# Optimization experiments

Measured on AMD Instinct MI355X. Metric: run time of the kernel, lower is better.

## Reference

```python
import jax, jax.numpy as jnp
import numpy as np

N_NODES = 50000
N_EDGES = 800000
D_IN = 256
H = 4
D_OUT = 64
NEG_SLOPE = 0.2


def setup_inputs() -> dict:
    key = jax.random.key(0)
    ks = jax.random.split(key, 6)
    feat = jax.random.normal(ks[0], (N_NODES, D_IN), dtype=jnp.float32)
    src = jax.random.randint(ks[1], (N_EDGES,), 0, N_NODES, dtype=jnp.int32)
    dst = jax.random.randint(ks[2], (N_EDGES,), 0, N_NODES, dtype=jnp.int32)
    # Glorot-ish scaled params
    W_src = jax.random.normal(ks[3], (H * D_OUT, D_IN), dtype=jnp.float32) * (1.0 / np.sqrt(D_IN))
    W_dst = jax.random.normal(ks[4], (H * D_OUT, D_IN), dtype=jnp.float32) * (1.0 / np.sqrt(D_IN))
    b_src = jnp.zeros((H * D_OUT,), dtype=jnp.float32)
    b_dst = jnp.zeros((H * D_OUT,), dtype=jnp.float32)
    attn = jax.random.normal(ks[5], (H, D_OUT), dtype=jnp.float32) * (1.0 / np.sqrt(D_OUT))
    return {"feat": feat, "src": src, "dst": dst, "W_src": W_src, "b_src": b_src,
            "W_dst": W_dst, "b_dst": b_dst, "attn": attn}


def reference(feat, src, dst, W_src, b_src, W_dst, b_dst, attn):
    n = feat.shape[0]
    h, d = attn.shape
    # node projections [N, H, D]
    feat_src = (feat @ W_src.T + b_src).reshape(n, h, d)
    feat_dst = (feat @ W_dst.T + b_dst).reshape(n, h, d)
    # edge-wise u + v, LeakyReLU  -> [E, H, D]
    e = jax.nn.leaky_relu(feat_src[src] + feat_dst[dst], negative_slope=NEG_SLOPE)
    # attention logits [E, H]
    score = jnp.einsum('ehd,hd->eh', e, attn)
    # edge softmax over incoming edges per dst node (numerically stable)
    m = jax.ops.segment_max(score, dst, num_segments=n)
    expv = jnp.exp(score - m[dst])
    denom = jax.ops.segment_sum(expv, dst, num_segments=n)
    a = expv / denom[dst]  # [E, H]
    # weighted scatter-sum of source features -> [N, H, D]
    out = jax.ops.segment_sum(feat_src[src] * a[:, :, None], dst, num_segments=n)
    return out
```

## Files before the change

### kernel.cpp

```cpp
#include <hip/hip_runtime.h>
#include <math.h>

#define N_DIN 256
#define N_COUT 256
#define NEG_SLOPE 0.2f
#define L2E 1.44269504f
#define CAP 64

#define BM 128
#define BN 256
#define BK 32
#define LDK 40

typedef _Float16 f16;
typedef f16 f16x2 __attribute__((ext_vector_type(2)));
typedef f16 f16x4 __attribute__((ext_vector_type(4)));
typedef f16 f16x8 __attribute__((ext_vector_type(8)));
typedef float f32x4 __attribute__((ext_vector_type(4)));
typedef float f32x8 __attribute__((ext_vector_type(8)));

__global__ __launch_bounds__(512) void proj(
    const float* __restrict__ feat,
    const float* __restrict__ Wsrc, const float* __restrict__ bsrc,
    const float* __restrict__ Wdst, const float* __restrict__ bdst,
    f16* __restrict__ fsrc_h, f16* __restrict__ fdst_h, int n)
{
    __shared__ f16 Al[BM * LDK];
    __shared__ f16 Bl[BN * LDK];

    const int t = threadIdx.x;
    const int lane = t & 63;
    const int w = t >> 6;
    const int wr = w >> 2, wc = w & 3;
    const int which = blockIdx.x & 1;
    const float* __restrict__ W    = which ? Wdst : Wsrc;
    const float* __restrict__ bias = which ? bdst : bsrc;
    f16* __restrict__ outp         = which ? fdst_h : fsrc_h;
    const int row0 = ((int)blockIdx.x >> 1) * BM;

    const int lr = lane & 15;
    const int kc = lane >> 4;

    const int arow = t >> 2;
    const int akof = (t & 3) * 8;
    const int bcol = t >> 1;
    const int bkof = (t & 1) * 16;
    const int agrow = row0 + arow;
    const bool aval = agrow < n;
    const float* __restrict__ fbase = &feat[(size_t)(aval ? agrow : 0) * N_DIN];
    const float* __restrict__ wbase = &W[(size_t)bcol * N_DIN];

    f32x4 acc[4][4] = {};

    for (int k0 = 0; k0 < N_DIN; k0 += BK) {
        {
            f16x8 v = {};
            if (aval) {
                const float* fp = fbase + k0 + akof;
                float4 u0 = *reinterpret_cast<const float4*>(fp);
                float4 u1 = *reinterpret_cast<const float4*>(fp + 4);
                v[0] = (f16)u0.x; v[1] = (f16)u0.y; v[2] = (f16)u0.z; v[3] = (f16)u0.w;
                v[4] = (f16)u1.x; v[5] = (f16)u1.y; v[6] = (f16)u1.z; v[7] = (f16)u1.w;
            }
            *reinterpret_cast<f16x8*>(&Al[arow * LDK + akof]) = v;
        }
        {
            const float* wp = wbase + k0 + bkof;
            float4 u0 = *reinterpret_cast<const float4*>(wp);
            float4 u1 = *reinterpret_cast<const float4*>(wp + 4);
            float4 u2 = *reinterpret_cast<const float4*>(wp + 8);
            float4 u3 = *reinterpret_cast<const float4*>(wp + 12);
            f16x8 v0, v1;
            v0[0] = (f16)u0.x; v0[1] = (f16)u0.y; v0[2] = (f16)u0.z; v0[3] = (f16)u0.w;
            v0[4] = (f16)u1.x; v0[5] = (f16)u1.y; v0[6] = (f16)u1.z; v0[7] = (f16)u1.w;
            v1[0] = (f16)u2.x; v1[1] = (f16)u2.y; v1[2] = (f16)u2.z; v1[3] = (f16)u2.w;
            v1[4] = (f16)u3.x; v1[5] = (f16)u3.y; v1[6] = (f16)u3.z; v1[7] = (f16)u3.w;
            *reinterpret_cast<f16x8*>(&Bl[bcol * LDK + bkof]) = v0;
            *reinterpret_cast<f16x8*>(&Bl[bcol * LDK + bkof + 8]) = v1;
        }
        __syncthreads();

        f16x8 a[4], b[4];
        #pragma unroll
        for (int nf = 0; nf < 4; ++nf)
            a[nf] = *reinterpret_cast<const f16x8*>(
                &Bl[(wc * 64 + nf * 16 + lr) * LDK + kc * 8]);
        #pragma unroll
        for (int m = 0; m < 4; ++m)
            b[m] = *reinterpret_cast<const f16x8*>(
                &Al[(wr * 64 + m * 16 + lr) * LDK + kc * 8]);
        #pragma unroll
        for (int nf = 0; nf < 4; ++nf)
            #pragma unroll
            for (int m = 0; m < 4; ++m)
                acc[nf][m] = __builtin_amdgcn_mfma_f32_16x16x32_f16(
                    a[nf], b[m], acc[nf][m], 0, 0, 0);
        __syncthreads();
    }

    #pragma unroll
    for (int nf = 0; nf < 4; ++nf) {
        const int cbase = wc * 64 + nf * 16 + kc * 4;
        const float4 bv = *reinterpret_cast<const float4*>(&bias[cbase]);
        #pragma unroll
        for (int m = 0; m < 4; ++m) {
            const int row = row0 + wr * 64 + m * 16 + lr;
            if (row < n) {
                f16x4 o;
                o[0] = (f16)(acc[nf][m][0] + bv.x);
                o[1] = (f16)(acc[nf][m][1] + bv.y);
                o[2] = (f16)(acc[nf][m][2] + bv.z);
                o[3] = (f16)(acc[nf][m][3] + bv.w);
                *reinterpret_cast<f16x4*>(&outp[(size_t)row * N_COUT + cbase]) = o;
            }
        }
    }
}


__global__ __launch_bounds__(1024) void histA(
    const int* __restrict__ dst, int* __restrict__ hist, int E, int NB, int NGRP)
{
    __shared__ int cnt[256];
    const int b = blockIdx.x, t = threadIdx.x;
    if (t < 256) cnt[t] = 0;
    __syncthreads();
    int i = b * 1024 + t;
    if (i < E) atomicAdd(&cnt[dst[i] >> 8], 1);
    __syncthreads();
    if (t < NGRP) hist[(size_t)t * NB + b] = cnt[t];
}

__global__ __launch_bounds__(1024) void scanA(
    int* __restrict__ hist, int* __restrict__ gtot, int NB)
{
    __shared__ int wsum[16];
    int* h = hist + (size_t)blockIdx.x * NB;
    const int t = threadIdx.x, lane = t & 63, wv = t >> 6;
    int v = (t < NB) ? h[t] : 0;
    int x = v;
    #pragma unroll
    for (int o = 1; o < 64; o <<= 1) {
        int y = __shfl_up(x, (unsigned)o);
        if (lane >= o) x += y;
    }
    if (lane == 63) wsum[wv] = x;
    __syncthreads();
    if (t < 16) {
        int s = wsum[t];
        #pragma unroll
        for (int o = 1; o < 16; o <<= 1) {
            int y = __shfl_up(s, (unsigned)o);
            if (t >= o) s += y;
        }
        wsum[t] = s;
    }
    __syncthreads();
    int wbase = wv ? wsum[wv - 1] : 0;
    if (t < NB) h[t] = wbase + x - v;
    if (t == 0) gtot[blockIdx.x] = wsum[15];
}

__global__ __launch_bounds__(256) void scanB(
    const int* __restrict__ gtot, int* __restrict__ gbase, int NGRP, int E)
{
    __shared__ int wsum[4];
    const int t = threadIdx.x, lane = t & 63, wv = t >> 6;
    int v = (t < NGRP) ? gtot[t] : 0;
    int x = v;
    #pragma unroll
    for (int o = 1; o < 64; o <<= 1) {
        int y = __shfl_up(x, (unsigned)o);
        if (lane >= o) x += y;
    }
    if (lane == 63) wsum[wv] = x;
    __syncthreads();
    if (t < 4) {
        int s = wsum[t];
        #pragma unroll
        for (int o = 1; o < 4; o <<= 1) {
            int y = __shfl_up(s, (unsigned)o);
            if (t >= o) s += y;
        }
        wsum[t] = s;
    }
    __syncthreads();
    int wbase = wv ? wsum[wv - 1] : 0;
    if (t < NGRP) gbase[t] = wbase + x - v;
    if (t == 0) gbase[NGRP] = E;
}

__global__ __launch_bounds__(1024) void partition(
    const int* __restrict__ src, const int* __restrict__ dst,
    const int* __restrict__ hist, const int* __restrict__ gbase,
    int* __restrict__ psrc, int* __restrict__ pdst, int E, int NB, int NGRP)
{
    __shared__ int cnt[256];
    const int b = blockIdx.x, t = threadIdx.x;
    if (t < 256) cnt[t] = 0;
    __syncthreads();
    int i = b * 1024 + t;
    if (i < E) {
        int d = dst[i];
        int s = src[i];
        int g = d >> 8;
        int lr = atomicAdd(&cnt[g], 1);
        int pos = gbase[g] + hist[(size_t)g * NB + b] + lr;
        pdst[pos] = d;
        psrc[pos] = s;
    }
}

__global__ __launch_bounds__(1024) void finebucket(
    const int* __restrict__ psrc, const int* __restrict__ pdst,
    const int* __restrict__ gbase, int* __restrict__ ssrc,
    int* __restrict__ deg, int n)
{
    __shared__ int cnt[256];
    const int g = blockIdx.x, t = threadIdx.x;
    if (t < 256) cnt[t] = 0;
    __syncthreads();
    const int beg = gbase[g], end = gbase[g + 1];
    for (int i = beg + t; i < end; i += 1024) {
        int d = pdst[i];
        int s = psrc[i];
        int r = atomicAdd(&cnt[d & 255], 1);
        if (r < CAP) ssrc[(size_t)d * CAP + r] = s;
    }
    __syncthreads();
    int d = (g << 8) + t;
    if (t < 256 && d < n) deg[d] = cnt[t];
}


template<int Q>
__device__ __forceinline__ void gat_batch(
    int e0, int i0m, int i1m,
    const f16* __restrict__ fsrc_h, int cb,
    f16x8 fd, f16x8 aw, f16x8 zz, f16x8 slp,
    float& l, f32x8& acc)
{
    f16x8 fr[Q];
    #pragma unroll
    for (int q = 0; q < Q; ++q) {
        int e = e0 + q;
        int u = __shfl((e < 32) ? i0m : i1m, e & 31, 32);
        fr[q] = *reinterpret_cast<const f16x8*>(&fsrc_h[(size_t)u * N_COUT + cb]);
    }
    float s[Q];
    #pragma unroll
    for (int q = 0; q < Q; ++q) {
        f16x8 x = fr[q] + fd;
        f16x8 e = slp * __builtin_elementwise_min(x, zz)
                + __builtin_elementwise_max(x, zz);
        f16x2 e0v = { e[0], e[1] }, e1v = { e[2], e[3] };
        f16x2 e2v = { e[4], e[5] }, e3v = { e[6], e[7] };
        f16x2 a0 = { aw[0], aw[1] }, a1 = { aw[2], aw[3] };
        f16x2 a2 = { aw[4], aw[5] }, a3 = { aw[6], aw[7] };
        s[q] = __builtin_amdgcn_fdot2(e3v, a3,
                __builtin_amdgcn_fdot2(e2v, a2,
                 __builtin_amdgcn_fdot2(e1v, a1,
                  __builtin_amdgcn_fdot2(e0v, a0, 0.f, false), false), false), false);
    }
    #pragma unroll
    for (int o = 1; o < 8; o <<= 1) {
        #pragma unroll
        for (int q = 0; q < Q; ++q) s[q] += __shfl_xor(s[q], o);
    }
    float ls = 0.f;
    #pragma unroll
    for (int q = 0; q < Q; ++q) {
        float p = exp2f(s[q]);
        #pragma unroll
        for (int k = 0; k < 8; ++k)
            acc[k] = fmaf((float)fr[q][k], p, acc[k]);
        ls += p;
    }
    l += ls;
}

__global__ __launch_bounds__(256) void gat16(
    const f16* __restrict__ fsrc_h, const f16* __restrict__ fdst_h,
    const float* __restrict__ attn, const int* __restrict__ deg,
    const int* __restrict__ ssrc, float* __restrict__ out, int n)
{
    const int t = threadIdx.x;
    const int v = blockIdx.x * 8 + (t >> 5);
    if (v >= n) return;
    const int lane = t & 31;
    const int cb = lane * 8;

    float4 aw0 = *reinterpret_cast<const float4*>(&attn[cb]);
    float4 aw1 = *reinterpret_cast<const float4*>(&attn[cb + 4]);
    f16x8 aw;
    aw[0] = (f16)(aw0.x * L2E); aw[1] = (f16)(aw0.y * L2E);
    aw[2] = (f16)(aw0.z * L2E); aw[3] = (f16)(aw0.w * L2E);
    aw[4] = (f16)(aw1.x * L2E); aw[5] = (f16)(aw1.y * L2E);
    aw[6] = (f16)(aw1.z * L2E); aw[7] = (f16)(aw1.w * L2E);
    const f16x8 zz = { (f16)0.f, (f16)0.f, (f16)0.f, (f16)0.f,
                       (f16)0.f, (f16)0.f, (f16)0.f, (f16)0.f };
    const f16x8 slp = { (f16)NEG_SLOPE, (f16)NEG_SLOPE, (f16)NEG_SLOPE, (f16)NEG_SLOPE,
                        (f16)NEG_SLOPE, (f16)NEG_SLOPE, (f16)NEG_SLOPE, (f16)NEG_SLOPE };

    f16x8 fd = *reinterpret_cast<const f16x8*>(&fdst_h[(size_t)v * N_COUT + cb]);

    int cnt = deg[v];
    if (cnt > CAP) cnt = CAP;
    const int base = v * CAP;

    int i0m = ssrc[base + lane];
    int i1m = ssrc[base + 32 + lane];

    float l = 0.f;
    f32x8 acc = {};

    int i = 0;
    for (; i + 8 <= cnt; i += 8)
        gat_batch<8>(i, i0m, i1m, fsrc_h, cb, fd, aw, zz, slp, l, acc);
    if (i + 4 <= cnt) {
        gat_batch<4>(i, i0m, i1m, fsrc_h, cb, fd, aw, zz, slp, l, acc);
        i += 4;
    }
    for (; i < cnt; ++i)
        gat_batch<1>(i, i0m, i1m, fsrc_h, cb, fd, aw, zz, slp, l, acc);

    const float inv = (l > 0.f) ? (1.0f / l) : 0.f;
    #pragma unroll
    for (int k = 0; k < 8; ++k) acc[k] *= inv;
    *reinterpret_cast<f32x8*>(&out[(size_t)v * N_COUT + cb]) = acc;
}

extern "C" void kernel_launch(void* const* d_in, const int* in_sizes, int n_in,
                              void* d_out, int out_size, void* d_ws, size_t ws_size,
                              hipStream_t stream)
{
    const float* feat = (const float*)d_in[0];
    const int*   src  = (const int*)d_in[1];
    const int*   dst  = (const int*)d_in[2];
    const float* Wsrc = (const float*)d_in[3];
    const float* bsrc = (const float*)d_in[4];
    const float* Wdst = (const float*)d_in[5];
    const float* bdst = (const float*)d_in[6];
    const float* attn = (const float*)d_in[7];

    const int N = in_sizes[0] / N_DIN;
    const int E = in_sizes[1];
    float* out = (float*)d_out;

    const int NB   = (E + 1023) / 1024;
    const int NGRP = (N + 255) >> 8;

    char* ws = (char*)d_ws;
    f16* fsrc_h = (f16*)ws; ws += (size_t)N * N_COUT * sizeof(f16);
    f16* fdst_h = (f16*)ws; ws += (size_t)N * N_COUT * sizeof(f16);
    int* psrc   = (int*)ws; ws += (size_t)E * sizeof(int);
    int* pdst   = (int*)ws; ws += (size_t)E * sizeof(int);
    int* hist   = (int*)ws; ws += (size_t)NGRP * NB * sizeof(int);
    int* gtot   = (int*)ws; ws += (size_t)(NGRP + 16) * sizeof(int);
    int* gbase  = (int*)ws; ws += (size_t)(NGRP + 16) * sizeof(int);
    int* deg    = (int*)ws; ws += (size_t)N * sizeof(int);
    int* ssrc   = (int*)ws; ws += (size_t)N * CAP * sizeof(int);

    const int ngemm = 2 * ((N + BM - 1) / BM);

    proj<<<ngemm, 512, 0, stream>>>(feat, Wsrc, bsrc, Wdst, bdst, fsrc_h, fdst_h, N);

    histA<<<NB, 1024, 0, stream>>>(dst, hist, E, NB, NGRP);
    scanA<<<NGRP, 1024, 0, stream>>>(hist, gtot, NB);
    scanB<<<1, 256, 0, stream>>>(gtot, gbase, NGRP, E);
    partition<<<NB, 1024, 0, stream>>>(src, dst, hist, gbase, psrc, pdst, E, NB, NGRP);
    finebucket<<<NGRP, 1024, 0, stream>>>(psrc, pdst, gbase, ssrc, deg, N);

    gat16<<<(N + 7) / 8, 256, 0, stream>>>(fsrc_h, fdst_h, attn, deg, ssrc, out, N);
}
```

Measured before the change: 157.6 us.

## Pre-convert weights to fp16 and restructure projection GEMM to read feat once

Adds a small kernel that converts both weight matrices to fp16 once per call. The projection kernel now computes both src and dst projections for a 64-row tile in one block, so each feat row is read once instead of twice. Weight fragments are loaded straight from global/L2 instead of staging through LDS, and the feat tile uses a double-buffered LDS with register prefetch and a single barrier per k-step. The risk is more L2 traffic for weight fragments and smaller tiles per block.

New measurement: 158.4 us. About the same (+0.5%).

```diff
diff --git a/kernel.cpp b/kernel.cpp
--- a/kernel.cpp
+++ b/kernel.cpp
@@ -7,10 +7,7 @@
 #define L2E 1.44269504f
 #define CAP 64
 
-#define BM 128
-#define BN 256
-#define BK 32
-#define LDK 40
+#define LDK2 40
 
 typedef _Float16 f16;
 typedef f16 f16x2 __attribute__((ext_vector_type(2)));
@@ -19,92 +16,90 @@
 typedef float f32x4 __attribute__((ext_vector_type(4)));
 typedef float f32x8 __attribute__((ext_vector_type(8)));
 
-__global__ __launch_bounds__(512) void proj(
+__global__ __launch_bounds__(256) void prep2(
+    const float* __restrict__ Wsrc, const float* __restrict__ Wdst,
+    f16* __restrict__ wsrc_h, f16* __restrict__ wdst_h)
+{
+    const int b = blockIdx.x;
+    const float* __restrict__ in = (b < 32) ? Wsrc : Wdst;
+    f16* __restrict__ out        = (b < 32) ? wsrc_h : wdst_h;
+    size_t i = (size_t)(b & 31) * 2048 + (size_t)threadIdx.x * 8;
+    float4 v0 = *reinterpret_cast<const float4*>(&in[i]);
+    float4 v1 = *reinterpret_cast<const float4*>(&in[i + 4]);
+    f16x8 o;
+    o[0] = (f16)v0.x; o[1] = (f16)v0.y; o[2] = (f16)v0.z; o[3] = (f16)v0.w;
+    o[4] = (f16)v1.x; o[5] = (f16)v1.y; o[6] = (f16)v1.z; o[7] = (f16)v1.w;
+    *reinterpret_cast<f16x8*>(&out[i]) = o;
+}
+
+__global__ __launch_bounds__(512) void proj2(
     const float* __restrict__ feat,
-    const float* __restrict__ Wsrc, const float* __restrict__ bsrc,
-    const float* __restrict__ Wdst, const float* __restrict__ bdst,
+    const f16* __restrict__ wsrc_h, const float* __restrict__ bsrc,
+    const f16* __restrict__ wdst_h, const float* __restrict__ bdst,
     f16* __restrict__ fsrc_h, f16* __restrict__ fdst_h, int n)
 {
-    __shared__ f16 Al[BM * LDK];
-    __shared__ f16 Bl[BN * LDK];
+    __shared__ f16 Al[2][64 * LDK2];
 
     const int t = threadIdx.x;
     const int lane = t & 63;
     const int w = t >> 6;
-    const int wr = w >> 2, wc = w & 3;
-    const int which = blockIdx.x & 1;
-    const float* __restrict__ W    = which ? Wdst : Wsrc;
+    const int which = w >> 2;
+    const int col0 = (w & 3) * 64;
+    const f16* __restrict__ Wm     = which ? wdst_h : wsrc_h;
     const float* __restrict__ bias = which ? bdst : bsrc;
     f16* __restrict__ outp         = which ? fdst_h : fsrc_h;
-    const int row0 = ((int)blockIdx.x >> 1) * BM;
+    const int row0 = (int)blockIdx.x * 64;
 
     const int lr = lane & 15;
     const int kc = lane >> 4;
 
-    const int arow = t >> 2;
-    const int akof = (t & 3) * 8;
-    const int bcol = t >> 1;
-    const int bkof = (t & 1) * 16;
-    const int agrow = row0 + arow;
-    const bool aval = agrow < n;
-    const float* __restrict__ fbase = &feat[(size_t)(aval ? agrow : 0) * N_DIN];
-    const float* __restrict__ wbase = &W[(size_t)bcol * N_DIN];
+    const int arow = t >> 3;
+    const int akof = (t & 7) * 4;
+    int agrow = row0 + arow;
+    if (agrow >= n) agrow = n - 1;
+    const float* __restrict__ fbase = &feat[(size_t)agrow * N_DIN + akof];
 
     f32x4 acc[4][4] = {};
 
-    for (int k0 = 0; k0 < N_DIN; k0 += BK) {
-        {
-            f16x8 v = {};
-            if (aval) {
-                const float* fp = fbase + k0 + akof;
-                float4 u0 = *reinterpret_cast<const float4*>(fp);
-                float4 u1 = *reinterpret_cast<const float4*>(fp + 4);
-                v[0] = (f16)u0.x; v[1] = (f16)u0.y; v[2] = (f16)u0.z; v[3] = (f16)u0.w;
-                v[4] = (f16)u1.x; v[5] = (f16)u1.y; v[6] = (f16)u1.z; v[7] = (f16)u1.w;
-            }
-            *reinterpret_cast<f16x8*>(&Al[arow * LDK + akof]) = v;
-        }
-        {
-            const float* wp = wbase + k0 + bkof;
-            float4 u0 = *reinterpret_cast<const float4*>(wp);
-            float4 u1 = *reinterpret_cast<const float4*>(wp + 4);
-            float4 u2 = *reinterpret_cast<const float4*>(wp + 8);
-            float4 u3 = *reinterpret_cast<const float4*>(wp + 12);
-            f16x8 v0, v1;
-            v0[0] = (f16)u0.x; v0[1] = (f16)u0.y; v0[2] = (f16)u0.z; v0[3] = (f16)u0.w;
-            v0[4] = (f16)u1.x; v0[5] = (f16)u1.y; v0[6] = (f16)u1.z; v0[7] = (f16)u1.w;
-            v1[0] = (f16)u2.x; v1[1] = (f16)u2.y; v1[2] = (f16)u2.z; v1[3] = (f16)u2.w;
-            v1[4] = (f16)u3.x; v1[5] = (f16)u3.y; v1[6] = (f16)u3.z; v1[7] = (f16)u3.w;
-            *reinterpret_cast<f16x8*>(&Bl[bcol * LDK + bkof]) = v0;
-            *reinterpret_cast<f16x8*>(&Bl[bcol * LDK + bkof + 8]) = v1;
-        }
+    float4 pf = *reinterpret_cast<const float4*>(fbase);
+    int p = 0;
+
+    #pragma unroll
+    for (int ks = 0; ks < 8; ++ks) {
+        const int k0 = ks * 32;
+        float4 nx;
+        if (ks < 7) nx = *reinterpret_cast<const float4*>(fbase + k0 + 32);
+        f16x4 av;
+        av[0] = (f16)pf.x; av[1] = (f16)pf.y; av[2] = (f16)pf.z; av[3] = (f16)pf.w;
+        *reinterpret_cast<f16x4*>(&Al[p][arow * LDK2 + akof]) = av;
         __syncthreads();
 
-        f16x8 a[4], b[4];
+        f16x8 bfr[4], afr[4];
         #pragma unroll
         for (int nf = 0; nf < 4; ++nf)
-            a[nf] = *reinterpret_cast<const f16x8*>(
-                &Bl[(wc * 64 + nf * 16 + lr) * LDK + kc * 8]);
+            bfr[nf] = *reinterpret_cast<const f16x8*>(
+                &Wm[(size_t)(col0 + nf * 16 + lr) * N_DIN + k0 + kc * 8]);
         #pragma unroll
         for (int m = 0; m < 4; ++m)
-            b[m] = *reinterpret_cast<const f16x8*>(
-                &Al[(wr * 64 + m * 16 + lr) * LDK + kc * 8]);
+            afr[m] = *reinterpret_cast<const f16x8*>(
+                &Al[p][(m * 16 + lr) * LDK2 + kc * 8]);
         #pragma unroll
         for (int nf = 0; nf < 4; ++nf)
             #pragma unroll
             for (int m = 0; m < 4; ++m)
                 acc[nf][m] = __builtin_amdgcn_mfma_f32_16x16x32_f16(
-                    a[nf], b[m], acc[nf][m], 0, 0, 0);
-        __syncthreads();
+                    bfr[nf], afr[m], acc[nf][m], 0, 0, 0);
+        pf = nx;
+        p ^= 1;
     }
 
     #pragma unroll
     for (int nf = 0; nf < 4; ++nf) {
-        const int cbase = wc * 64 + nf * 16 + kc * 4;
+        const int cbase = col0 + nf * 16 + kc * 4;
         const float4 bv = *reinterpret_cast<const float4*>(&bias[cbase]);
         #pragma unroll
         for (int m = 0; m < 4; ++m) {
-            const int row = row0 + wr * 64 + m * 16 + lr;
+            const int row = row0 + m * 16 + lr;
             if (row < n) {
                 f16x4 o;
                 o[0] = (f16)(acc[nf][m][0] + bv.x);
@@ -117,7 +112,6 @@
     }
 }
 
-
 __global__ __launch_bounds__(1024) void histA(
     const int* __restrict__ dst, int* __restrict__ hist, int E, int NB, int NGRP)
 {
@@ -231,7 +225,6 @@
     int d = (g << 8) + t;
     if (t < 256 && d < n) deg[d] = cnt[t];
 }
-
 
 template<int Q>
 __device__ __forceinline__ void gat_batch(
@@ -351,6 +344,8 @@
     const int NGRP = (N + 255) >> 8;
 
     char* ws = (char*)d_ws;
+    f16* wsrc_h = (f16*)ws; ws += (size_t)N_COUT * N_DIN * sizeof(f16);
+    f16* wdst_h = (f16*)ws; ws += (size_t)N_COUT * N_DIN * sizeof(f16);
     f16* fsrc_h = (f16*)ws; ws += (size_t)N * N_COUT * sizeof(f16);
     f16* fdst_h = (f16*)ws; ws += (size_t)N * N_COUT * sizeof(f16);
     int* psrc   = (int*)ws; ws += (size_t)E * sizeof(int);
@@ -361,9 +356,10 @@
     int* deg    = (int*)ws; ws += (size_t)N * sizeof(int);
     int* ssrc   = (int*)ws; ws += (size_t)N * CAP * sizeof(int);
 
-    const int ngemm = 2 * ((N + BM - 1) / BM);
-
-    proj<<<ngemm, 512, 0, stream>>>(feat, Wsrc, bsrc, Wdst, bdst, fsrc_h, fdst_h, N);
+    prep2<<<64, 256, 0, stream>>>(Wsrc, Wdst, wsrc_h, wdst_h);
+
+    proj2<<<(N + 63) / 64, 512, 0, stream>>>(feat, wsrc_h, bsrc, wdst_h, bdst,
+                                             fsrc_h, fdst_h, N);
 
     histA<<<NB, 1024, 0, stream>>>(dst, hist, E, NB, NGRP);
     scanA<<<NGRP, 1024, 0, stream>>>(hist, gtot, NB);
```
